# Optimization experiments

Hardware: AMD Instinct MI355X
Metric: run time of the kernel (lower is better)

The kernel has to match this reference:

```python
import jax, jax.numpy as jnp
import numpy as np

THRESHOLD = 0.05
TOP_N = 512
NMS_THR = 0.6
POST_TOP_N = 100
MIN_SIZE = 0.0
N_CLASS = 8
IMG_SIZE = (256.0, 256.0, 64.0)
B, C, H, W, D = 4, 8, 128, 128, 32


def _pairwise_iou3d(b):
    # b: [K, 6] in xyzxyz; returns [K, K] volumetric IoU
    lo, hi = b[:, :3], b[:, 3:]
    ilo = jnp.maximum(lo[:, None, :], lo[None, :, :])
    ihi = jnp.minimum(hi[:, None, :], hi[None, :, :])
    inter = jnp.prod(jnp.maximum(ihi - ilo, 0.0), axis=-1)
    vol = jnp.prod(jnp.maximum(hi - lo, 0.0), axis=-1)
    return inter / (vol[:, None] + vol[None, :] - inter + 1e-9)


def _nms_keep(boxes, scores, thr):
    # greedy NMS; scores == -1 marks invalid entries. Returns bool keep mask [K].
    K = boxes.shape[0]
    order = jnp.argsort(-scores)
    b = boxes[order]
    s = scores[order]
    iou = _pairwise_iou3d(b)
    idx = jnp.arange(K)

    def body(i, keep):
        sup = (iou[i] > thr) & keep[i] & (idx > i)
        return keep & ~sup

    keep = jax.lax.fori_loop(0, K, body, s > 0.0)
    return jnp.zeros(K, dtype=bool).at[order].set(keep)


def _forward(location, cls_pred, box_pred, center_pred):
    Bb, Cc = cls_pred.shape[0], cls_pred.shape[1]
    N = cls_pred.shape[2] * cls_pred.shape[3] * cls_pred.shape[4]
    # [B, C, H, W, D] -> [B, N, C]
    cls = jax.nn.sigmoid(cls_pred).transpose(0, 2, 3, 4, 1).reshape(Bb, N, Cc)
    ctr = jax.nn.sigmoid(center_pred).transpose(0, 2, 3, 4, 1).reshape(Bb, N)
    box = box_pred.transpose(0, 2, 3, 4, 1).reshape(Bb, N, 6)

    candid = cls > THRESHOLD                      # [B, N, C]
    scores = cls * ctr[:, :, None]                # centerness-weighted
    flat = jnp.where(candid, scores, -1.0).reshape(Bb, N * Cc)
    vals, idx = jax.lax.top_k(flat, TOP_N)        # fixed-size stand-in for mask+topk
    valid = vals > 0.0                            # matches torch clamp(count, top_n)

    loc_idx = idx // Cc                           # flattened spatial location
    class_id = idx % Cc + 1                       # labels are 1-based
    bsel = jnp.take_along_axis(box, loc_idx[..., None], axis=1)   # [B, K, 6]
    lsel = location[loc_idx]                                      # [B, K, 3]
    det = jnp.concatenate([lsel - bsel[..., :3], lsel + bsel[..., 3:]], axis=-1)

    # BoxList.clip to image volume
    full = jnp.concatenate([jnp.asarray(IMG_SIZE), jnp.asarray(IMG_SIZE)]).astype(det.dtype) - 1.0
    det = jnp.clip(det, 0.0, full)

    score = jnp.where(valid, jnp.sqrt(jnp.where(valid, vals, 1.0)), 0.0)

    # remove_small_boxes
    sides = det[..., 3:] - det[..., :3]
    valid = valid & jnp.all(sides >= MIN_SIZE, axis=-1)

    # per-class greedy NMS (decisions are non-differentiable; torch detaches anyway)
    det_ng = jax.lax.stop_gradient(det)
    score_ng = jax.lax.stop_gradient(score)

    def per_image(b_i, s_i, c_i, v_i):
        def per_class(j):
            m = v_i & (c_i == j)
            return _nms_keep(b_i, jnp.where(m, s_i, -1.0), NMS_THR) & m
        return jnp.any(jax.vmap(per_class)(jnp.arange(1, N_CLASS + 1)), axis=0)

    valid = jax.vmap(per_image)(det_ng, score_ng, class_id, valid)

    # post_top_n selection (kthvalue threshold == keep top post_top_n scores)
    fv, fi = jax.lax.top_k(jnp.where(valid, score_ng, -1.0), POST_TOP_N)
    fvalid = fv > 0.0
    fbox = jnp.take_along_axis(det, fi[..., None], axis=1) * fvalid[..., None]
    fscore = jnp.where(fvalid, jnp.take_along_axis(score, fi, axis=1), 0.0)
    flabel = jnp.where(fvalid, jnp.take_along_axis(class_id, fi, axis=1), 0)
    return fbox, fscore, flabel, fvalid


def setup_inputs() -> dict:
    key = jax.random.key(0)
    k1, k2, k3, k4 = jax.random.split(key, 4)
    N = H * W * D
    location = jax.random.uniform(k1, (N, 3), dtype=jnp.float32) * jnp.asarray(IMG_SIZE, jnp.float32)
    cls_pred = jax.random.normal(k2, (B, C, H, W, D), dtype=jnp.float32) - 2.0  # realistic logits
    box_pred = jax.random.uniform(k3, (B, 6, H, W, D), dtype=jnp.float32) * 20.0  # positive extents
    center_pred = jax.random.normal(k4, (B, 1, H, W, D), dtype=jnp.float32)
    return {"location": location, "cls_pred": cls_pred, "box_pred": box_pred, "center_pred": center_pred}


def reference(location, cls_pred, box_pred, center_pred):
    return _forward(location, cls_pred, box_pred, center_pred)
```

## Files before the change

kernel.cpp:

```cpp
#include <hip/hip_runtime.h>

#define NB 4
#define NC 8
#define NLOC 524288
#define TOPN 512
#define POST 100
#define NBIN 8192
#define SELBINS 4096
#define SCAP 4096
#define CAP 16384
#define KPT 16
#define LCAP 2048
#define NMS_THR 0.6f
#define CAND_THR 0.05f
#define SPEC_THR 0.5f

typedef unsigned long long ull;

#define OFF_CNT    0
#define OFF_OVF    16
#define OFF_KEYS   64
#define ZERO_BYTES 32

__device__ __forceinline__ float sigmoidf_(float x) {
    return 1.0f / (1.0f + __expf(-x));
}

__global__ __launch_bounds__(256) void gather_spec(const float* __restrict__ cls,
                                                   const float* __restrict__ ctr,
                                                   ull* __restrict__ keys,
                                                   unsigned int* __restrict__ counts,
                                                   unsigned int* __restrict__ ovf) {
    __shared__ ull lkeys[LCAP];
    __shared__ unsigned int lcnt;
    __shared__ unsigned int lbase;
    const int b = blockIdx.y;
    if (threadIdx.x == 0) lcnt = 0;
    __syncthreads();

    const int n0 = (blockIdx.x * blockDim.x + threadIdx.x) * 8;
    const float4* cvp = (const float4*)(ctr + (size_t)b * NLOC + n0);
    const float4 cv0 = cvp[0], cv1 = cvp[1];
    float4 cl0[NC], cl1[NC];
    #pragma unroll
    for (int c = 0; c < NC; ++c) {
        const float4* p = (const float4*)(cls + ((size_t)b * NC + c) * NLOC + n0);
        cl0[c] = p[0];
        cl1[c] = p[1];
    }

    #pragma unroll
    for (int h = 0; h < 2; ++h) {
        const float4 cv = h ? cv1 : cv0;
        #pragma unroll
        for (int j = 0; j < 4; ++j) {
            bool any = false;
            #pragma unroll
            for (int c = 0; c < NC; ++c) {
                const float x = h ? ((const float*)&cl1[c])[j] : ((const float*)&cl0[c])[j];
                any |= (x > 0.0f);
            }
            if (any) {
                const float sc = sigmoidf_(((const float*)&cv)[j]);
                #pragma unroll
                for (int c = 0; c < NC; ++c) {
                    const float x = h ? ((const float*)&cl1[c])[j] : ((const float*)&cl0[c])[j];
                    if (x > 0.0f) {
                        const float p = sigmoidf_(x) * sc;
                        if (p > SPEC_THR) {
                            const unsigned pos = atomicAdd(&lcnt, 1u);
                            if (pos < LCAP) {
                                const unsigned flat = (unsigned)((n0 + h * 4 + j) * NC + c);
                                lkeys[pos] = ((ull)__float_as_uint(p) << 32) | (unsigned)(~flat);
                            }
                        }
                    }
                }
            }
        }
    }
    __syncthreads();
    const unsigned m = lcnt;
    if (threadIdx.x == 0) {
        const unsigned stored = (m > LCAP) ? LCAP : m;
        lbase = atomicAdd(&counts[b], stored);
        if (m > LCAP) ovf[b] = 1;
    }
    __syncthreads();
    const unsigned stored = (m > LCAP) ? LCAP : m;
    const unsigned base = lbase;
    for (unsigned i = threadIdx.x; i < stored; i += blockDim.x) {
        const unsigned pos = base + i;
        if (pos < CAP) keys[(size_t)b * CAP + pos] = lkeys[i];
    }
}

__device__ __forceinline__ float iou3d_(const float* a, const float* bx) {
    const float ix = fminf(a[3], bx[3]) - fmaxf(a[0], bx[0]);
    const float iy = fminf(a[4], bx[4]) - fmaxf(a[1], bx[1]);
    const float iz = fminf(a[5], bx[5]) - fmaxf(a[2], bx[2]);
    const float inter = fmaxf(ix, 0.0f) * fmaxf(iy, 0.0f) * fmaxf(iz, 0.0f);
    const float v0 = fmaxf(a[3] - a[0], 0.0f) * fmaxf(a[4] - a[1], 0.0f) * fmaxf(a[5] - a[2], 0.0f);
    const float v1 = fmaxf(bx[3] - bx[0], 0.0f) * fmaxf(bx[4] - bx[1], 0.0f) * fmaxf(bx[5] - bx[2], 0.0f);
    return inter / (v0 + v1 - inter + 1e-9f);
}

__global__ __launch_bounds__(1024) void select_nms_kernel(const float* __restrict__ cls,
                                                          const float* __restrict__ ctr,
                                                          ull* __restrict__ keys,
                                                          unsigned int* __restrict__ counts,
                                                          const unsigned int* __restrict__ ovf,
                                                          const float* __restrict__ loc,
                                                          const float* __restrict__ box,
                                                          float* __restrict__ out) {
    __shared__ union SU {
        struct { unsigned int hist[SELBINS]; ull surv[SCAP]; } sel;
        unsigned int fhist[NBIN];
        struct { float sd[TOPN * 6]; float ss[TOPN]; int scl[TOPN];
                 int keep[TOPN]; int clist[NC][TOPN]; int wcnt[NC]; } nms;
    } u;
    __shared__ ull tk[TOPN];
    __shared__ unsigned int scnt;
    __shared__ int cut_s;

    const int b = blockIdx.x, t = threadIdx.x;

    {
        const unsigned cnt0 = counts[b];
        const bool bad = !(cnt0 >= TOPN && cnt0 <= CAP && ovf[b] == 0);
        if (bad) {
            for (int i = t; i < NBIN; i += 1024) u.fhist[i] = 0;
            __syncthreads();
            for (int n = t; n < NLOC; n += 1024) {
                const float sc = sigmoidf_(ctr[(size_t)b * NLOC + n]);
                #pragma unroll
                for (int c = 0; c < NC; ++c) {
                    const float s = sigmoidf_(cls[((size_t)b * NC + c) * NLOC + n]);
                    if (s > CAND_THR) atomicAdd(&u.fhist[__float_as_uint(s * sc) >> 17], 1u);
                }
            }
            __syncthreads();
            if (t == 0) {
                unsigned cum = 0; int bin = 0;
                for (int i = NBIN - 1; i >= 0; --i) {
                    cum += u.fhist[i];
                    if (cum >= TOPN) { bin = i; break; }
                }
                cut_s = bin;
                counts[b] = 0;
            }
            __syncthreads();
            const unsigned cb2 = (unsigned)cut_s;
            for (int n = t; n < NLOC; n += 1024) {
                const float sc = sigmoidf_(ctr[(size_t)b * NLOC + n]);
                #pragma unroll
                for (int c = 0; c < NC; ++c) {
                    const float s = sigmoidf_(cls[((size_t)b * NC + c) * NLOC + n]);
                    if (s > CAND_THR) {
                        const unsigned bits = __float_as_uint(s * sc);
                        if ((bits >> 17) >= cb2) {
                            const unsigned pos = atomicAdd(&counts[b], 1u);
                            if (pos < CAP)
                                keys[(size_t)b * CAP + pos] =
                                    ((ull)bits << 32) | (unsigned)(~(unsigned)(n * NC + c));
                        }
                    }
                }
            }
            __threadfence();
        }
    }
    __syncthreads();

    const int M = (int)min(counts[b], (unsigned)CAP);

    ull kr[KPT];
    {
        const ulonglong2* kb = (const ulonglong2*)(keys + (size_t)b * CAP);
        #pragma unroll
        for (int p = 0; p < KPT / 2; ++p) {
            const ulonglong2 v = kb[p * 1024 + t];
            kr[2 * p] = v.x;
            kr[2 * p + 1] = v.y;
        }
    }

    for (int i = t; i < SELBINS; i += 1024) u.sel.hist[i] = 0;
    if (t == 0) scnt = 0;
    if (t < TOPN) tk[t] = 0;
    __syncthreads();
    #pragma unroll
    for (int p = 0; p < KPT / 2; ++p) {
        #pragma unroll
        for (int q = 0; q < 2; ++q) {
            const int i = 2 * (p * 1024 + t) + q;
            if (i < M) {
                const unsigned hi = (unsigned)(kr[2 * p + q] >> 32);
                const int off = (int)hi - 0x3F000000;
                int bin = (off < 0) ? 0 : (off >> 11);
                if (bin > SELBINS - 1) bin = SELBINS - 1;
                atomicAdd(&u.sel.hist[bin], 1u);
            }
        }
    }
    __syncthreads();

    if (t < 64) {
        unsigned s = 0;
        for (int i = 0; i < 64; ++i)
            s += u.sel.hist[t * 64 + ((i + t) & 63)];
        unsigned suf = s;
        #pragma unroll
        for (int d = 1; d < 64; d <<= 1) {
            const unsigned o = __shfl_down(suf, d);
            suf += (t + d < 64) ? o : 0u;
        }
        const ull mask = __ballot(suf >= TOPN);
        unsigned nxt = __shfl_down(suf, 1);
        if (t == 63) nxt = 0;
        if (mask == 0ull) {
            if (t == 0) cut_s = 0;
        } else {
            const int L = 63 - __builtin_clzll(mask);
            if (t == L) {
                unsigned cum = nxt;
                int c = L * 64;
                for (int i = 63; i >= 0; --i) {
                    cum += u.sel.hist[L * 64 + i];
                    if (cum >= TOPN) { c = L * 64 + i; break; }
                }
                cut_s = c;
            }
        }
    }
    __syncthreads();

    const int cb = cut_s;
    #pragma unroll
    for (int p = 0; p < KPT / 2; ++p) {
        #pragma unroll
        for (int q = 0; q < 2; ++q) {
            const int i = 2 * (p * 1024 + t) + q;
            if (i < M) {
                const ull k = kr[2 * p + q];
                const unsigned hi = (unsigned)(k >> 32);
                const int off = (int)hi - 0x3F000000;
                int bin = (off < 0) ? 0 : (off >> 11);
                if (bin > SELBINS - 1) bin = SELBINS - 1;
                if (bin >= cb) {
                    const unsigned p2 = atomicAdd(&scnt, 1u);
                    if (p2 < SCAP) u.sel.surv[p2] = k;
                }
            }
        }
    }
    __syncthreads();

    const unsigned sc_final = scnt;
    if (sc_final <= (unsigned)SCAP) {
        const int S = (int)sc_final;
        for (int i = t; i < S; i += 1024) {
            const ull ke = u.sel.surv[i];
            int r = 0;
            for (int j = 0; j < S; ++j) r += (u.sel.surv[j] > ke) ? 1 : 0;
            if (r < TOPN) tk[r] = ke;
        }
    } else {
        for (int i = t; i < M; i += 1024) {
            const ull ke = keys[(size_t)b * CAP + i];
            int r = 0;
            for (int j = 0; j < M; ++j) r += (keys[(size_t)b * CAP + j] > ke) ? 1 : 0;
            if (r < TOPN) tk[r] = ke;
        }
    }
    __syncthreads();

    if (t < TOPN) {
        const ull k = tk[t];
        const unsigned bits = (unsigned)(k >> 32);
        const float val = __uint_as_float(bits);
        int valid = (val > 0.0f) ? 1 : 0;
        const unsigned flat = ~(unsigned)(k & 0xffffffffu);
        int n = 0, c = 0;
        if (valid) { n = (int)(flat >> 3); c = (int)(flat & 7u); }
        const float lx = loc[n * 3 + 0], ly = loc[n * 3 + 1], lz = loc[n * 3 + 2];
        const float* bp = box + (size_t)b * 6 * NLOC + n;
        const float b0 = bp[0];
        const float b1 = bp[(size_t)NLOC];
        const float b2 = bp[2 * (size_t)NLOC];
        const float b3 = bp[3 * (size_t)NLOC];
        const float b4 = bp[4 * (size_t)NLOC];
        const float b5 = bp[5 * (size_t)NLOC];
        const float d0 = fminf(fmaxf(lx - b0, 0.0f), 255.0f);
        const float d1 = fminf(fmaxf(ly - b1, 0.0f), 255.0f);
        const float d2 = fminf(fmaxf(lz - b2, 0.0f), 63.0f);
        const float d3 = fminf(fmaxf(lx + b3, 0.0f), 255.0f);
        const float d4 = fminf(fmaxf(ly + b4, 0.0f), 255.0f);
        const float d5 = fminf(fmaxf(lz + b5, 0.0f), 63.0f);
        if (d3 - d0 < 0.0f || d4 - d1 < 0.0f || d5 - d2 < 0.0f) valid = 0;
        u.nms.sd[t * 6 + 0] = d0; u.nms.sd[t * 6 + 1] = d1; u.nms.sd[t * 6 + 2] = d2;
        u.nms.sd[t * 6 + 3] = d3; u.nms.sd[t * 6 + 4] = d4; u.nms.sd[t * 6 + 5] = d5;
        u.nms.ss[t] = (val > 0.0f) ? sqrtf(val) : 0.0f;
        u.nms.scl[t] = c + 1;
        u.nms.keep[t] = valid;
    }
    __syncthreads();

    if (t < TOPN) {
        const int w = t >> 6, lane = t & 63;
        const int myclass = w + 1;
        int cnt = 0;
        for (int j0 = 0; j0 < TOPN; j0 += 64) {
            const int j = j0 + lane;
            const bool pred = (u.nms.scl[j] == myclass) && (u.nms.keep[j] != 0);
            const ull m = __ballot(pred);
            if (pred) {
                const int pos = cnt + __popcll(m & ((1ull << lane) - 1ull));
                u.nms.clist[w][pos] = j;
            }
            cnt += __popcll(m);
        }
        __threadfence_block();

        if (cnt <= 128) {
            const int g0 = (lane < cnt) ? u.nms.clist[w][lane] : -1;
            const int g1 = (lane + 64 < cnt) ? u.nms.clist[w][lane + 64] : -1;
            float B0[6], B1[6];
            #pragma unroll
            for (int q = 0; q < 6; ++q) {
                B0[q] = (g0 >= 0) ? u.nms.sd[g0 * 6 + q] : 0.0f;
                B1[q] = (g1 >= 0) ? u.nms.sd[g1 * 6 + q] : 0.0f;
            }
            bool a0 = (g0 >= 0), a1 = (g1 >= 0);
            ull m0 = __ballot(a0), m1 = __ballot(a1);
            for (int i = 0; i < cnt; ++i) {
                const int ki = i >> 6, li = i & 63;
                const ull mi = ki ? m1 : m0;
                if (!((mi >> li) & 1ull)) continue;
                float pb[6];
                #pragma unroll
                for (int q = 0; q < 6; ++q) pb[q] = __shfl(ki ? B1[q] : B0[q], li);
                if (a0 && lane > i)      { if (iou3d_(B0, pb) > NMS_THR) a0 = false; }
                if (a1 && lane + 64 > i) { if (iou3d_(B1, pb) > NMS_THR) a1 = false; }
                m0 = __ballot(a0); m1 = __ballot(a1);
            }
            if (g0 >= 0 && !a0) u.nms.keep[g0] = 0;
            if (g1 >= 0 && !a1) u.nms.keep[g1] = 0;
        } else {
            volatile int* vkeep = u.nms.keep;
            const float* sd = u.nms.sd;
            for (int i = 0; i < cnt; ++i) {
                const int gi = u.nms.clist[w][i];
                if (!vkeep[gi]) continue;
                float pb[6];
                #pragma unroll
                for (int q = 0; q < 6; ++q) pb[q] = sd[gi * 6 + q];
                for (int e = i + 1 + lane; e < cnt; e += 64) {
                    const int gj = u.nms.clist[w][e];
                    if (vkeep[gj]) {
                        float cb_[6];
                        #pragma unroll
                        for (int q = 0; q < 6; ++q) cb_[q] = sd[gj * 6 + q];
                        if (iou3d_(cb_, pb) > NMS_THR) vkeep[gj] = 0;
                    }
                }
                __threadfence_block();
            }
        }
    }
    __syncthreads();

    if (t < TOPN) {
        const int w = t >> 6, lane = t & 63;
        const ull km = __ballot(u.nms.keep[t] != 0);
        if (lane == 0) u.nms.wcnt[w] = __popcll(km);
    }
    __syncthreads();
    if (t < TOPN) {
        const int w = t >> 6, lane = t & 63;
        const ull km = __ballot(u.nms.keep[t] != 0);
        int before = 0, total = 0;
        #pragma unroll
        for (int w2 = 0; w2 < NC; ++w2) {
            total += u.nms.wcnt[w2];
            if (w2 < w) before += u.nms.wcnt[w2];
        }
        const int myrank = before + __popcll(km & ((1ull << lane) - 1ull));

        float* fbox = out;
        float* fscore = out + NB * POST * 6;
        float* flabel = out + NB * POST * 7;
        float* fvalid = out + NB * POST * 8;

        if (u.nms.keep[t] && myrank < POST) {
            #pragma unroll
            for (int k = 0; k < 6; ++k) fbox[(b * POST + myrank) * 6 + k] = u.nms.sd[t * 6 + k];
            fscore[b * POST + myrank] = u.nms.ss[t];
            flabel[b * POST + myrank] = (float)u.nms.scl[t];
            fvalid[b * POST + myrank] = 1.0f;
        }
        const int tc = (total < POST) ? total : POST;
        if (t >= tc && t < POST) {
            #pragma unroll
            for (int k = 0; k < 6; ++k) fbox[(b * POST + t) * 6 + k] = 0.0f;
            fscore[b * POST + t] = 0.0f;
            flabel[b * POST + t] = 0.0f;
            fvalid[b * POST + t] = 0.0f;
        }
    }
}

extern "C" void kernel_launch(void* const* d_in, const int* in_sizes, int n_in,
                              void* d_out, int out_size, void* d_ws, size_t ws_size,
                              hipStream_t stream) {
    const float* location = (const float*)d_in[0];
    const float* cls_pred = (const float*)d_in[1];
    const float* box_pred = (const float*)d_in[2];
    const float* ctr_pred = (const float*)d_in[3];

    char* ws = (char*)d_ws;
    unsigned int* counts = (unsigned int*)(ws + OFF_CNT);
    unsigned int* ovf    = (unsigned int*)(ws + OFF_OVF);
    ull*          keys   = (ull*)(ws + OFF_KEYS);

    hipMemsetAsync(d_ws, 0, ZERO_BYTES, stream);

    gather_spec<<<dim3(NLOC / 2048, NB), 256, 0, stream>>>(cls_pred, ctr_pred, keys, counts, ovf);
    select_nms_kernel<<<NB, 1024, 0, stream>>>(cls_pred, ctr_pred, keys, counts, ovf,
                                               location, box_pred, (float*)d_out);
}
```

Before: 85.96 us.

## Precompute per-class IoU bitmasks, aggregate survivor atomics per wave, skip unused key loads

Several changes land together in the select+NMS kernel. Survivor compaction now uses one atomicAdd per wavefront via ballot and popcount instead of one per thread. Key loads past M are skipped, and the tk zero-fill only covers the unwritten tail. The rank-count loop is unrolled. The small-class NMS path first computes a suppression bitmask per lane from boxes compacted per class in shared memory, so the serial greedy loop only tests bits instead of doing shuffles and IoU each iteration. The cost is more shared memory for the compacted boxes and IoU computed for every pair, including pairs whose suppressor was already removed.

```diff
diff --git a/kernel.cpp b/kernel.cpp
--- a/kernel.cpp
+++ b/kernel.cpp
@@ -117,13 +117,15 @@
         struct { unsigned int hist[SELBINS]; ull surv[SCAP]; } sel;
         unsigned int fhist[NBIN];
         struct { float sd[TOPN * 6]; float ss[TOPN]; int scl[TOPN];
-                 int keep[TOPN]; int clist[NC][TOPN]; int wcnt[NC]; } nms;
+                 int keep[TOPN]; int clist[NC][TOPN];
+                 float cbox[NC][128][6]; int wcnt[NC]; } nms;
     } u;
     __shared__ ull tk[TOPN];
     __shared__ unsigned int scnt;
     __shared__ int cut_s;
 
     const int b = blockIdx.x, t = threadIdx.x;
+    const int lane = t & 63;
 
     {
         const unsigned cnt0 = counts[b];
@@ -179,7 +181,9 @@
         const ulonglong2* kb = (const ulonglong2*)(keys + (size_t)b * CAP);
         #pragma unroll
         for (int p = 0; p < KPT / 2; ++p) {
-            const ulonglong2 v = kb[p * 1024 + t];
+            const int vi = p * 1024 + t;
+            ulonglong2 v; v.x = 0; v.y = 0;
+            if (2 * vi < M) v = kb[vi];
             kr[2 * p] = v.x;
             kr[2 * p + 1] = v.y;
         }
@@ -187,7 +191,6 @@
 
     for (int i = t; i < SELBINS; i += 1024) u.sel.hist[i] = 0;
     if (t == 0) scnt = 0;
-    if (t < TOPN) tk[t] = 0;
     __syncthreads();
     #pragma unroll
     for (int p = 0; p < KPT / 2; ++p) {
@@ -207,6 +210,7 @@
 
     if (t < 64) {
         unsigned s = 0;
+        #pragma unroll 8
         for (int i = 0; i < 64; ++i)
             s += u.sel.hist[t * 64 + ((i + t) & 63)];
         unsigned suf = s;
@@ -241,16 +245,22 @@
         #pragma unroll
         for (int q = 0; q < 2; ++q) {
             const int i = 2 * (p * 1024 + t) + q;
+            const ull k = kr[2 * p + q];
+            bool pred = false;
             if (i < M) {
-                const ull k = kr[2 * p + q];
                 const unsigned hi = (unsigned)(k >> 32);
                 const int off = (int)hi - 0x3F000000;
                 int bin = (off < 0) ? 0 : (off >> 11);
                 if (bin > SELBINS - 1) bin = SELBINS - 1;
-                if (bin >= cb) {
-                    const unsigned p2 = atomicAdd(&scnt, 1u);
-                    if (p2 < SCAP) u.sel.surv[p2] = k;
-                }
+                pred = (bin >= cb);
+            }
+            const ull mv = __ballot(pred);
+            unsigned base = 0;
+            if (lane == 0 && mv) base = atomicAdd(&scnt, (unsigned)__popcll(mv));
+            base = __shfl(base, 0);
+            if (pred) {
+                const unsigned pos = base + (unsigned)__popcll(mv & ((1ull << lane) - 1ull));
+                if (pos < SCAP) u.sel.surv[pos] = k;
             }
         }
     }
@@ -262,9 +272,15 @@
         for (int i = t; i < S; i += 1024) {
             const ull ke = u.sel.surv[i];
             int r = 0;
-            for (int j = 0; j < S; ++j) r += (u.sel.surv[j] > ke) ? 1 : 0;
+            int j = 0;
+            for (; j + 16 <= S; j += 16) {
+                #pragma unroll
+                for (int qq = 0; qq < 16; ++qq) r += (u.sel.surv[j + qq] > ke) ? 1 : 0;
+            }
+            for (; j < S; ++j) r += (u.sel.surv[j] > ke) ? 1 : 0;
             if (r < TOPN) tk[r] = ke;
         }
+        for (int r = S + t; r < TOPN; r += 1024) tk[r] = 0;
     } else {
         for (int i = t; i < M; i += 1024) {
             const ull ke = keys[(size_t)b * CAP + i];
@@ -272,6 +288,8 @@
             for (int j = 0; j < M; ++j) r += (keys[(size_t)b * CAP + j] > ke) ? 1 : 0;
             if (r < TOPN) tk[r] = ke;
         }
+        const int W = (M < TOPN) ? M : TOPN;
+        for (int r = W + t; r < TOPN; r += 1024) tk[r] = 0;
     }
     __syncthreads();
 
@@ -307,7 +325,7 @@
     __syncthreads();
 
     if (t < TOPN) {
-        const int w = t >> 6, lane = t & 63;
+        const int w = t >> 6;
         const int myclass = w + 1;
         int cnt = 0;
         for (int j0 = 0; j0 < TOPN; j0 += 64) {
@@ -317,50 +335,64 @@
             if (pred) {
                 const int pos = cnt + __popcll(m & ((1ull << lane) - 1ull));
                 u.nms.clist[w][pos] = j;
+                if (pos < 128) {
+                    #pragma unroll
+                    for (int q = 0; q < 6; ++q) u.nms.cbox[w][pos][q] = u.nms.sd[j * 6 + q];
+                }
             }
             cnt += __popcll(m);
         }
         __threadfence_block();
 
         if (cnt <= 128) {
-            const int g0 = (lane < cnt) ? u.nms.clist[w][lane] : -1;
-            const int g1 = (lane + 64 < cnt) ? u.nms.clist[w][lane + 64] : -1;
-            float B0[6], B1[6];
+            const bool h0 = (lane < cnt), h1 = (lane + 64 < cnt);
+            float A0[6], A1[6];
             #pragma unroll
             for (int q = 0; q < 6; ++q) {
-                B0[q] = (g0 >= 0) ? u.nms.sd[g0 * 6 + q] : 0.0f;
-                B1[q] = (g1 >= 0) ? u.nms.sd[g1 * 6 + q] : 0.0f;
-            }
-            bool a0 = (g0 >= 0), a1 = (g1 >= 0);
+                A0[q] = h0 ? u.nms.cbox[w][lane][q] : 0.0f;
+                A1[q] = h1 ? u.nms.cbox[w][lane + 64][q] : 0.0f;
+            }
+            ull s0 = 0, s1lo = 0, s1hi = 0;
+            #pragma unroll 2
+            for (int i = 0; i < cnt; ++i) {
+                float pb[6];
+                #pragma unroll
+                for (int q = 0; q < 6; ++q) pb[q] = u.nms.cbox[w][i][q];
+                if (i < 64) {
+                    if (h0 && lane > i && iou3d_(A0, pb) > NMS_THR) s0 |= 1ull << i;
+                    if (h1 && iou3d_(A1, pb) > NMS_THR) s1lo |= 1ull << i;
+                } else {
+                    if (h1 && (i - 64) < lane && iou3d_(A1, pb) > NMS_THR) s1hi |= 1ull << (i - 64);
+                }
+            }
+            bool a0 = h0, a1 = h1;
             ull m0 = __ballot(a0), m1 = __ballot(a1);
             for (int i = 0; i < cnt; ++i) {
-                const int ki = i >> 6, li = i & 63;
-                const ull mi = ki ? m1 : m0;
-                if (!((mi >> li) & 1ull)) continue;
-                float pb[6];
-                #pragma unroll
-                for (int q = 0; q < 6; ++q) pb[q] = __shfl(ki ? B1[q] : B0[q], li);
-                if (a0 && lane > i)      { if (iou3d_(B0, pb) > NMS_THR) a0 = false; }
-                if (a1 && lane + 64 > i) { if (iou3d_(B1, pb) > NMS_THR) a1 = false; }
+                const bool alive_i = (i < 64) ? ((m0 >> i) & 1ull) : ((m1 >> (i - 64)) & 1ull);
+                if (!alive_i) continue;
+                if (a0 && i < 64 && ((s0 >> i) & 1ull)) a0 = false;
+                if (a1) {
+                    const bool sb = (i < 64) ? ((s1lo >> i) & 1ull) : ((s1hi >> (i - 64)) & 1ull);
+                    if (sb) a1 = false;
+                }
                 m0 = __ballot(a0); m1 = __ballot(a1);
             }
-            if (g0 >= 0 && !a0) u.nms.keep[g0] = 0;
-            if (g1 >= 0 && !a1) u.nms.keep[g1] = 0;
+            if (h0 && !a0) u.nms.keep[u.nms.clist[w][lane]] = 0;
+            if (h1 && !a1) u.nms.keep[u.nms.clist[w][lane + 64]] = 0;
         } else {
             volatile int* vkeep = u.nms.keep;
-            const float* sd = u.nms.sd;
             for (int i = 0; i < cnt; ++i) {
                 const int gi = u.nms.clist[w][i];
                 if (!vkeep[gi]) continue;
                 float pb[6];
                 #pragma unroll
-                for (int q = 0; q < 6; ++q) pb[q] = sd[gi * 6 + q];
+                for (int q = 0; q < 6; ++q) pb[q] = u.nms.sd[gi * 6 + q];
                 for (int e = i + 1 + lane; e < cnt; e += 64) {
                     const int gj = u.nms.clist[w][e];
                     if (vkeep[gj]) {
                         float cb_[6];
                         #pragma unroll
-                        for (int q = 0; q < 6; ++q) cb_[q] = sd[gj * 6 + q];
+                        for (int q = 0; q < 6; ++q) cb_[q] = u.nms.sd[gj * 6 + q];
                         if (iou3d_(cb_, pb) > NMS_THR) vkeep[gj] = 0;
                     }
                 }
@@ -371,13 +403,13 @@
     __syncthreads();
 
     if (t < TOPN) {
-        const int w = t >> 6, lane = t & 63;
+        const int w = t >> 6;
         const ull km = __ballot(u.nms.keep[t] != 0);
         if (lane == 0) u.nms.wcnt[w] = __popcll(km);
     }
     __syncthreads();
     if (t < TOPN) {
-        const int w = t >> 6, lane = t & 63;
+        const int w = t >> 6;
         const ull km = __ballot(u.nms.keep[t] != 0);
         int before = 0, total = 0;
         #pragma unroll
```

Measured after the change: 88.24 us. +2.7%, slower.
